# Kernel optimization log

Measured on AMD Instinct MI355X. Metric: run time of the kernel, lower is better.

## Reference

```python
import jax, jax.numpy as jnp
import numpy as np

K, D, O, B = 65536, 256, 256, 1024

def setup_inputs() -> dict:
    key = jax.random.key(0)
    k1, k2, k3 = jax.random.split(key, 3)
    return {
        "x": jax.random.normal(k1, (B, D), dtype=jnp.float32),
        "mean": jax.random.normal(k2, (K, D), dtype=jnp.float32),
        "stddev": jnp.ones((K, D), dtype=jnp.float32),
        "outputs": jax.random.normal(k3, (K, O), dtype=jnp.float32),
        "top_k": 32,
    }

def reference(x, mean, stddev, outputs, top_k):
    # Joint Gaussian log-prob summed over feature dim, computed without the
    # [B, K, D] broadcast torch materializes. Expanding sum_d ((x-mu)/sigma)^2
    # gives three GEMM-shaped terms.
    d = x.shape[-1]
    inv_var = 1.0 / (stddev * stddev)                      # [K, D]
    quad = ((x * x) @ inv_var.T                            # [B, K]
            - 2.0 * (x @ (mean * inv_var).T)
            + jnp.sum(mean * mean * inv_var, axis=-1))
    log_norm = jnp.sum(jnp.log(stddev), axis=-1) + 0.5 * d * jnp.log(2.0 * jnp.pi)
    joint_lp = -0.5 * quad - log_norm                      # [B, K]
    top_lp, top_idx = jax.lax.top_k(joint_lp, top_k)       # [B, top_k]
    weights = jax.nn.softmax(top_lp, axis=-1)              # [B, top_k]
    gathered = outputs[top_idx]                            # [B, top_k, O]
    return jnp.einsum('bko,bk->bo', gathered, weights)     # [B, O]
```

## Files before the change

### kernel.cpp

```cpp
#include <hip/hip_runtime.h>
#include <stdint.h>

#define KCOMP 65536
#define DDIM  256
#define ODIM  256
#define BROWS 1024
#define NCB   512
#define NBLK  512
#define LOG2PI_TERM 235.2482645f

typedef float f32x4 __attribute__((ext_vector_type(4)));
typedef __bf16 bf16x8 __attribute__((ext_vector_type(8)));
typedef unsigned int u32;
typedef unsigned long long u64;
typedef unsigned short u16;

typedef __attribute__((address_space(1))) const u32 gconst_u32;
typedef __attribute__((address_space(3))) u32 lds_u32;

__device__ __forceinline__ u16 f2bf(float f) {
  u32 b = __float_as_uint(f);
  b += 0x7FFFu + ((b >> 16) & 1u);
  return (u16)(b >> 16);
}
__device__ __forceinline__ u32 fkey(float f) {
  u32 b = __float_as_uint(f);
  return b ^ ((b >> 31) ? 0xFFFFFFFFu : 0x80000000u);
}

#define DPP_ROR1 0x121
#define DPP_ROR2 0x122
#define DPP_ROR4 0x124
#define DPP_ROR8 0x128

#define WS_A     0
#define WS_KEY   (1u << 20)

__global__ void prep_A(const float* __restrict__ x, u16* __restrict__ A) {
  int l = threadIdx.x & 63;
  int wv = threadIdx.x >> 6;
  int t = blockIdx.x;
  int row = t * 16 + (l & 15);
  for (int u = 0; u < 4; ++u) {
    int cc = wv * 4 + u;
    int d0 = cc * 16 + ((l >> 4) << 2);
    float4 xv = *(const float4*)(x + (size_t)row * DDIM + d0);
    float xs[4] = {xv.x, xv.y, xv.z, xv.w};
    uint4 v;
    u32 wds[4];
    for (int e = 0; e < 4; ++e)
      wds[e] = (u32)f2bf(xs[e] * xs[e]) | ((u32)f2bf(-2.0f * xs[e]) << 16);
    v.x = wds[0]; v.y = wds[1]; v.z = wds[2]; v.w = wds[3];
    *(uint4*)(A + ((size_t)(t * 16 + cc) * 64 + l) * 8) = v;
  }
}

__global__ __launch_bounds__(512, 4)
void main_gemm(const u16* __restrict__ A_ws, const float* __restrict__ mean,
               const float* __restrict__ stdd, u32* __restrict__ ckey) {
  __shared__ __align__(16) char lds_raw[66560];
  __shared__ u32 wsel[2][32][17];
  int tid = threadIdx.x, l = tid & 63, w = tid >> 6;
  int nb = blockIdx.x;
  int p = l & 15, q = l >> 4;

  u32 kid0 = (u32)(w * 16 + q * 4);

  bf16x8 wf[16];
  float myc0;
  f32x4 mycv;
  {
    u32* scr = (u32*)(lds_raw + w * 8320);
    int p8 = l & 7, q8 = l >> 3;
#pragma unroll
    for (int rr = 0; rr < 2; ++rr) {
      int comp = (nb * 8 + w) * 16 + rr * 8 + p8;
      const float* mrow = mean + (size_t)comp * DDIM + q8 * 32;
      const float* srow = stdd + (size_t)comp * DDIM + q8 * 32;
      float gsum = 0.f;
#pragma unroll
      for (int i = 0; i < 8; ++i) {
        float4 m4 = *(const float4*)(mrow + 4 * i);
        float4 s4 = *(const float4*)(srow + 4 * i);
        float ms[4] = {m4.x, m4.y, m4.z, m4.w};
        float ss[4] = {s4.x, s4.y, s4.z, s4.w};
        u32 wd[4];
#pragma unroll
        for (int e = 0; e < 4; ++e) {
          float iv = __builtin_amdgcn_rcpf(ss[e] * ss[e]);
          float miv = ms[e] * iv;
          wd[e] = (u32)f2bf(-0.5f * iv) | ((u32)f2bf(-0.5f * miv) << 16);
          gsum -= 0.5f * ms[e] * miv + __logf(ss[e]);
        }
        uint4 v; v.x = wd[0]; v.y = wd[1]; v.z = wd[2]; v.w = wd[3];
        *(uint4*)(scr + p8 * 260 + q8 * 32 + i * 4) = v;
      }
      gsum += __shfl_xor(gsum, 8);
      gsum += __shfl_xor(gsum, 16);
      gsum += __shfl_xor(gsum, 32);
      if ((p >> 3) == rr) {
        myc0 = gsum - LOG2PI_TERM;
#pragma unroll
        for (int cc = 0; cc < 16; ++cc)
          wf[cc] = *(const bf16x8*)(scr + (p & 7) * 260 + cc * 16 + q * 4);
      }
    }
#pragma unroll
    for (int i = 0; i < 4; ++i)
      mycv[i] = __shfl(myc0, q * 4 + i);
  }
  __syncthreads();

#define ASHP(B, CELL) (lds_raw + ((size_t)(B) * 32 + (CELL)) * 1024)

#define ISSUE(S, B)                                                           \
  {                                                                           \
    _Pragma("unroll")                                                         \
    for (int u = 0; u < 4; ++u) {                                             \
      int cell = w * 4 + u;                                                   \
      const u16* gsrc = A_ws +                                                \
        ((size_t)((S) * 2 + (cell >> 4)) * 16 + (cell & 15)) * 512            \
        + (size_t)l * 8;                                                      \
      __builtin_amdgcn_global_load_lds((gconst_u32*)gsrc,                     \
          (lds_u32*)ASHP(B, cell), 16, 0, 0);                                 \
    }                                                                         \
  }

#define MERGE_EMIT(ST, B)                                                     \
  {                                                                           \
    int r = tid;                                                              \
    u32 top[4] = {~0u, ~0u, ~0u, ~0u};                                        \
    _Pragma("unroll")                                                         \
    for (int j = 0; j < 16; ++j) {                                            \
      u32 key = wsel[B][r][j];                                                \
      if (key < top[3]) {                                                     \
        top[3] = key;                                                         \
        for (int z = 3; z > 0 && top[z] < top[z - 1]; --z) {                  \
          u32 tt = top[z]; top[z] = top[z - 1]; top[z - 1] = tt;              \
        }                                                                     \
      }                                                                       \
    }                                                                         \
    int rowg = (ST) * 32 + r;                                                 \
    uint4 ov; ov.x = ~top[0]; ov.y = ~top[1]; ov.z = ~top[2]; ov.w = ~top[3]; \
    *(uint4*)&ckey[((size_t)rowg * NCB + nb) * 4] = ov;                       \
  }

  ISSUE(0, 0)
  for (int s = 0; s < 32; ++s) {
    int pb = s & 1;
    __syncthreads();
    if (s < 31) ISSUE(s + 1, pb ^ 1)
    if (s > 0 && tid < 32) MERGE_EMIT(s - 1, pb ^ 1)

    f32x4 ac[2];
    ac[0] = mycv;
    ac[1] = mycv;
    __builtin_amdgcn_s_setprio(1);
#pragma unroll
    for (int cc = 0; cc < 16; ++cc) {
      bf16x8 a0 = *(const bf16x8*)(ASHP(pb, cc) + (size_t)l * 16);
      bf16x8 a1 = *(const bf16x8*)(ASHP(pb, 16 + cc) + (size_t)l * 16);
      ac[0] = __builtin_amdgcn_mfma_f32_16x16x32_bf16(wf[cc], a0, ac[0], 0, 0, 0);
      ac[1] = __builtin_amdgcn_mfma_f32_16x16x32_bf16(wf[cc], a1, ac[1], 0, 0, 0);
    }
    __builtin_amdgcn_s_setprio(0);

#define UMIN(a, b) ((a) < (b) ? (a) : (b))
#define UMAX(a, b) ((a) < (b) ? (b) : (a))
#pragma unroll
    for (int t = 0; t < 2; ++t) {
      u32 k0 = (__float_as_uint(ac[t][0]) & 0xFFFFFF00u) | (kid0 + 0);
      u32 k1 = (__float_as_uint(ac[t][1]) & 0xFFFFFF00u) | (kid0 + 1);
      u32 k2 = (__float_as_uint(ac[t][2]) & 0xFFFFFF00u) | (kid0 + 2);
      u32 k3 = (__float_as_uint(ac[t][3]) & 0xFFFFFF00u) | (kid0 + 3);
      u32 l0 = UMIN(k0, k1), h0 = UMAX(k0, k1);
      u32 l1 = UMIN(k2, k3), h1 = UMAX(k2, k3);
      u32 m1 = UMIN(l0, l1), m2 = UMIN(UMAX(l0, l1), UMIN(h0, h1));
      {
        u32 o1 = (u32)__shfl_xor((int)m1, 16);
        u32 o2 = (u32)__shfl_xor((int)m2, 16);
        u32 lo = UMIN(m1, o1), hi = UMAX(m1, o1), mn = UMIN(m2, o2);
        m1 = lo; m2 = UMIN(hi, mn);
      }
      {
        u32 o1 = (u32)__shfl_xor((int)m1, 32);
        u32 o2 = (u32)__shfl_xor((int)m2, 32);
        u32 lo = UMIN(m1, o1), hi = UMAX(m1, o1), mn = UMIN(m2, o2);
        m1 = lo; m2 = UMIN(hi, mn);
      }
      if (q == 0) {
        int r = t * 16 + p;
        wsel[pb][r][w * 2] = m1;
        wsel[pb][r][w * 2 + 1] = m2;
      }
    }
#undef UMIN
#undef UMAX
  }
  __syncthreads();
  if (tid < 32) MERGE_EMIT(31, 1)
#undef ISSUE
#undef MERGE_EMIT
#undef ASHP
}

__global__ __launch_bounds__(256)
void finalize(const float* __restrict__ x, const float* __restrict__ mean,
              const float* __restrict__ stdd, const float* __restrict__ outs,
              const u32* __restrict__ ckey, float* __restrict__ out) {
  __shared__ u32 cksh[2048];
  __shared__ float xr[256];
  __shared__ float part[256];
  __shared__ int selk[64];
  __shared__ float ew[32];
  __shared__ int kf[32];
  __shared__ float invs_sh;
  int tid = threadIdx.x, l = tid & 63, v = tid >> 6;
  int row = blockIdx.x;

  for (int i = tid; i < 2048; i += 256)
    cksh[i] = ckey[(size_t)row * 2048 + i];
  xr[tid] = x[(size_t)row * DDIM + tid];
  __syncthreads();

#define REDUCE_MAX(m)                                                         \
  {                                                                           \
    u32 o;                                                                    \
    o = (u32)__builtin_amdgcn_mov_dpp((int)m, DPP_ROR1, 0xf, 0xf, false);     \
    m = m > o ? m : o;                                                        \
    o = (u32)__builtin_amdgcn_mov_dpp((int)m, DPP_ROR2, 0xf, 0xf, false);     \
    m = m > o ? m : o;                                                        \
    o = (u32)__builtin_amdgcn_mov_dpp((int)m, DPP_ROR4, 0xf, 0xf, false);     \
    m = m > o ? m : o;                                                        \
    o = (u32)__builtin_amdgcn_mov_dpp((int)m, DPP_ROR8, 0xf, 0xf, false);     \
    m = m > o ? m : o;                                                        \
    o = (u32)__shfl_xor((int)m, 16); m = m > o ? m : o;                       \
    o = (u32)__shfl_xor((int)m, 32); m = m > o ? m : o;                       \
  }

  {
    u32 ext[8];
#pragma unroll
    for (int i = 0; i < 8; ++i) {
      int j = v * 512 + i * 64 + l;
      ext[i] = (cksh[j] & 0xFFFFFE00u) | ((u32)l << 3) | (u32)i;
    }
#define CSW(a, b) { if (ext[a] < ext[b]) { u32 t = ext[a]; ext[a] = ext[b]; ext[b] = t; } }
    CSW(0,1) CSW(2,3) CSW(4,5) CSW(6,7)
    CSW(0,2) CSW(1,3) CSW(4,6) CSW(5,7)
    CSW(1,2) CSW(5,6)
    CSW(0,4) CSW(1,5) CSW(2,6) CSW(3,7)
    CSW(2,4) CSW(3,5)
    CSW(1,2) CSW(3,4) CSW(5,6)
#undef CSW
    for (int it = 0; it < 16; ++it) {
      u32 m = ext[0];
      REDUCE_MAX(m)
      if (m == ext[0]) {
#pragma unroll
        for (int z = 0; z < 7; ++z) ext[z] = ext[z + 1];
        ext[7] = 0;
      }
      if (l == 0) {
        int wl = (int)((m >> 3) & 63u), wi = (int)(m & 7u);
        int j = v * 512 + wi * 64 + wl;
        selk[v * 16 + it] = (int)((u32)(j >> 2) * 128u + (~cksh[j] & 0x7Fu));
      }
    }
  }
  __syncthreads();

  {
    int j = tid >> 2, qq = tid & 3;
    int k = selk[j];
    const float* mr = mean + (size_t)k * DDIM + qq * 64;
    const float* sr = stdd + (size_t)k * DDIM + qq * 64;
    float s2 = 0.f, ls = 0.f;
    for (int i = 0; i < 16; ++i) {
      float4 m4 = *(const float4*)(mr + 4 * i);
      float4 s4 = *(const float4*)(sr + 4 * i);
      float4 x4 = *(const float4*)(&xr[qq * 64 + 4 * i]);
      { float is = 1.f / s4.x; float df = (x4.x - m4.x) * is; s2 += df * df; ls += __logf(s4.x); }
      { float is = 1.f / s4.y; float df = (x4.y - m4.y) * is; s2 += df * df; ls += __logf(s4.y); }
      { float is = 1.f / s4.z; float df = (x4.z - m4.z) * is; s2 += df * df; ls += __logf(s4.z); }
      { float is = 1.f / s4.w; float df = (x4.w - m4.w) * is; s2 += df * df; ls += __logf(s4.w); }
    }
    part[tid] = -0.5f * s2 - ls;
  }
  __syncthreads();

  if (tid < 64) {
    float lp0 = part[l * 4] + part[l * 4 + 1] + part[l * 4 + 2] +
                part[l * 4 + 3] - LOG2PI_TERM;
    u32 ext = (fkey(lp0) & 0xFFFFFFC0u) | (u32)l;
    float maxlp = 0.f, ssum = 0.f;
    for (int it = 0; it < 32; ++it) {
      u32 m = ext;
      REDUCE_MAX(m)
      int j = (int)(m & 63u);
      u32 vb = m & 0xFFFFFFC0u;
      vb ^= (vb >> 31) ? 0x80000000u : 0xFFFFFFFFu;
      float lp = __uint_as_float(vb);
      if (it == 0) maxlp = lp;
      float e = __expf(lp - maxlp);
      ssum += e;
      if (l == 0) { ew[it] = e; kf[it] = selk[j]; }
      if (j == l) ext = 0;
    }
    if (l == 0) invs_sh = 1.0f / ssum;
  }
  __syncthreads();
#undef REDUCE_MAX

  {
    float a = 0.f;
    for (int i = 0; i < 32; ++i)
      a += ew[i] * outs[(size_t)kf[i] * ODIM + tid];
    out[(size_t)row * ODIM + tid] = a * invs_sh;
  }
}

extern "C" void kernel_launch(void* const* d_in, const int* in_sizes, int n_in,
                              void* d_out, int out_size, void* d_ws, size_t ws_size,
                              hipStream_t stream) {
  const float* x = (const float*)d_in[0];
  const float* mean = (const float*)d_in[1];
  const float* stdd = (const float*)d_in[2];
  const float* outs = (const float*)d_in[3];
  char* ws = (char*)d_ws;
  u16* A_ws = (u16*)(ws + WS_A);
  u32* ckey = (u32*)(ws + WS_KEY);

  prep_A<<<64, 256, 0, stream>>>(x, A_ws);
  main_gemm<<<NBLK, 512, 0, stream>>>(A_ws, mean, stdd, ckey);
  finalize<<<BROWS, 256, 0, stream>>>(x, mean, stdd, outs, ckey,
                                      (float*)d_out);
}
```

Baseline: 379.7 us.

## Remap waves to 2x4 tile grid so each A fragment feeds two MFMAs

Waves are reorganised from 8 component groups times 2 row tiles into 2 row tiles times 4 component groups of 32 components each. Each wave now holds two sets of weight fragments and reuses one LDS A fragment for two MFMAs, halving LDS reads per MFMA. It also halves the per-row candidate count that the merge step scans. The cost is doubled weight-fragment registers, so launch bounds drop to 2 blocks per SM, lowering occupancy.

```diff
diff --git a/kernel.cpp b/kernel.cpp
--- a/kernel.cpp
+++ b/kernel.cpp
@@ -55,26 +55,29 @@
   }
 }
 
-__global__ __launch_bounds__(512, 4)
+__global__ __launch_bounds__(512, 2)
 void main_gemm(const u16* __restrict__ A_ws, const float* __restrict__ mean,
                const float* __restrict__ stdd, u32* __restrict__ ckey) {
   __shared__ __align__(16) char lds_raw[66560];
-  __shared__ u32 wsel[2][32][17];
+  __shared__ u32 wsel[2][32][9];
   int tid = threadIdx.x, l = tid & 63, w = tid >> 6;
   int nb = blockIdx.x;
   int p = l & 15, q = l >> 4;
-
-  u32 kid0 = (u32)(w * 16 + q * 4);
-
-  bf16x8 wf[16];
-  float myc0;
-  f32x4 mycv;
+  int wt = w >> 2;
+  int wc = w & 3;
+
+  u32 kid0 = (u32)(wc * 32 + q * 4);
+
+  bf16x8 wf[2][16];
+  float myc[2] = {0.f, 0.f};
+  f32x4 mycv[2];
   {
     u32* scr = (u32*)(lds_raw + w * 8320);
     int p8 = l & 7, q8 = l >> 3;
-#pragma unroll
-    for (int rr = 0; rr < 2; ++rr) {
-      int comp = (nb * 8 + w) * 16 + rr * 8 + p8;
+    int g0 = nb * 128 + wc * 32;
+#pragma unroll
+    for (int rr = 0; rr < 4; ++rr) {
+      int comp = g0 + rr * 8 + p8;
       const float* mrow = mean + (size_t)comp * DDIM + q8 * 32;
       const float* srow = stdd + (size_t)comp * DDIM + q8 * 32;
       float gsum = 0.f;
@@ -98,16 +101,21 @@
       gsum += __shfl_xor(gsum, 8);
       gsum += __shfl_xor(gsum, 16);
       gsum += __shfl_xor(gsum, 32);
-      if ((p >> 3) == rr) {
-        myc0 = gsum - LOG2PI_TERM;
-#pragma unroll
-        for (int cc = 0; cc < 16; ++cc)
-          wf[cc] = *(const bf16x8*)(scr + (p & 7) * 260 + cc * 16 + q * 4);
-      }
-    }
-#pragma unroll
-    for (int i = 0; i < 4; ++i)
-      mycv[i] = __shfl(myc0, q * 4 + i);
+#pragma unroll
+      for (int gs = 0; gs < 2; ++gs) {
+        if (((gs * 16 + p) >> 3) == rr) {
+          myc[gs] = gsum - LOG2PI_TERM;
+#pragma unroll
+          for (int cc = 0; cc < 16; ++cc)
+            wf[gs][cc] = *(const bf16x8*)(scr + (p & 7) * 260 + cc * 16 + q * 4);
+        }
+      }
+    }
+#pragma unroll
+    for (int gs = 0; gs < 2; ++gs)
+#pragma unroll
+      for (int i = 0; i < 4; ++i)
+        mycv[gs][i] = __shfl(myc[gs], q * 4 + i);
   }
   __syncthreads();
 
@@ -131,7 +139,7 @@
     int r = tid;                                                              \
     u32 top[4] = {~0u, ~0u, ~0u, ~0u};                                        \
     _Pragma("unroll")                                                         \
-    for (int j = 0; j < 16; ++j) {                                            \
+    for (int j = 0; j < 8; ++j) {                                             \
       u32 key = wsel[B][r][j];                                                \
       if (key < top[3]) {                                                     \
         top[3] = key;                                                         \
@@ -152,30 +160,43 @@
     if (s < 31) ISSUE(s + 1, pb ^ 1)
     if (s > 0 && tid < 32) MERGE_EMIT(s - 1, pb ^ 1)
 
-    f32x4 ac[2];
-    ac[0] = mycv;
-    ac[1] = mycv;
+    f32x4 ac0 = mycv[0];
+    f32x4 ac1 = mycv[1];
     __builtin_amdgcn_s_setprio(1);
 #pragma unroll
     for (int cc = 0; cc < 16; ++cc) {
-      bf16x8 a0 = *(const bf16x8*)(ASHP(pb, cc) + (size_t)l * 16);
-      bf16x8 a1 = *(const bf16x8*)(ASHP(pb, 16 + cc) + (size_t)l * 16);
-      ac[0] = __builtin_amdgcn_mfma_f32_16x16x32_bf16(wf[cc], a0, ac[0], 0, 0, 0);
-      ac[1] = __builtin_amdgcn_mfma_f32_16x16x32_bf16(wf[cc], a1, ac[1], 0, 0, 0);
+      bf16x8 a = *(const bf16x8*)(ASHP(pb, wt * 16 + cc) + (size_t)l * 16);
+      ac0 = __builtin_amdgcn_mfma_f32_16x16x32_bf16(wf[0][cc], a, ac0, 0, 0, 0);
+      ac1 = __builtin_amdgcn_mfma_f32_16x16x32_bf16(wf[1][cc], a, ac1, 0, 0, 0);
     }
     __builtin_amdgcn_s_setprio(0);
 
 #define UMIN(a, b) ((a) < (b) ? (a) : (b))
 #define UMAX(a, b) ((a) < (b) ? (b) : (a))
-#pragma unroll
-    for (int t = 0; t < 2; ++t) {
-      u32 k0 = (__float_as_uint(ac[t][0]) & 0xFFFFFF00u) | (kid0 + 0);
-      u32 k1 = (__float_as_uint(ac[t][1]) & 0xFFFFFF00u) | (kid0 + 1);
-      u32 k2 = (__float_as_uint(ac[t][2]) & 0xFFFFFF00u) | (kid0 + 2);
-      u32 k3 = (__float_as_uint(ac[t][3]) & 0xFFFFFF00u) | (kid0 + 3);
-      u32 l0 = UMIN(k0, k1), h0 = UMAX(k0, k1);
-      u32 l1 = UMIN(k2, k3), h1 = UMAX(k2, k3);
-      u32 m1 = UMIN(l0, l1), m2 = UMIN(UMAX(l0, l1), UMIN(h0, h1));
+    {
+      u32 a1_, a2_, b1_, b2_;
+      {
+        u32 k0 = (__float_as_uint(ac0[0]) & 0xFFFFFF00u) | (kid0 + 0);
+        u32 k1 = (__float_as_uint(ac0[1]) & 0xFFFFFF00u) | (kid0 + 1);
+        u32 k2 = (__float_as_uint(ac0[2]) & 0xFFFFFF00u) | (kid0 + 2);
+        u32 k3 = (__float_as_uint(ac0[3]) & 0xFFFFFF00u) | (kid0 + 3);
+        u32 l0 = UMIN(k0, k1), h0 = UMAX(k0, k1);
+        u32 l1 = UMIN(k2, k3), h1 = UMAX(k2, k3);
+        a1_ = UMIN(l0, l1);
+        a2_ = UMIN(UMAX(l0, l1), UMIN(h0, h1));
+      }
+      {
+        u32 k0 = (__float_as_uint(ac1[0]) & 0xFFFFFF00u) | (kid0 + 16);
+        u32 k1 = (__float_as_uint(ac1[1]) & 0xFFFFFF00u) | (kid0 + 17);
+        u32 k2 = (__float_as_uint(ac1[2]) & 0xFFFFFF00u) | (kid0 + 18);
+        u32 k3 = (__float_as_uint(ac1[3]) & 0xFFFFFF00u) | (kid0 + 19);
+        u32 l0 = UMIN(k0, k1), h0 = UMAX(k0, k1);
+        u32 l1 = UMIN(k2, k3), h1 = UMAX(k2, k3);
+        b1_ = UMIN(l0, l1);
+        b2_ = UMIN(UMAX(l0, l1), UMIN(h0, h1));
+      }
+      u32 m1 = UMIN(a1_, b1_);
+      u32 m2 = UMIN(UMAX(a1_, b1_), UMIN(a2_, b2_));
       {
         u32 o1 = (u32)__shfl_xor((int)m1, 16);
         u32 o2 = (u32)__shfl_xor((int)m2, 16);
@@ -189,9 +210,9 @@
         m1 = lo; m2 = UMIN(hi, mn);
       }
       if (q == 0) {
-        int r = t * 16 + p;
-        wsel[pb][r][w * 2] = m1;
-        wsel[pb][r][w * 2 + 1] = m2;
+        int r = wt * 16 + p;
+        wsel[pb][r][wc * 2] = m1;
+        wsel[pb][r][wc * 2 + 1] = m2;
       }
     }
 #undef UMIN
```

Result: slower. 391.1 us (+3.0%).

## Read GEMM A tiles directly from global memory instead of LDS double-buffering

Applied to the files above, without the earlier changes.

Removes the global_load_lds double-buffered staging of the component A tiles and has each wave load its bf16x8 MFMA operands straight from global memory (through L2/L1), replacing __syncthreads with a lighter lgkmcnt wait plus s_barrier. This drops the LDS traffic and full-block sync per stage, but loses explicit prefetch overlap, so MFMA issue may stall on global-load latency. The finalize kernel also swaps exact division for the hardware reciprocal approximation.

```diff
diff --git a/kernel.cpp b/kernel.cpp
--- a/kernel.cpp
+++ b/kernel.cpp
@@ -14,9 +14,6 @@
 typedef unsigned int u32;
 typedef unsigned long long u64;
 typedef unsigned short u16;
-
-typedef __attribute__((address_space(1))) const u32 gconst_u32;
-typedef __attribute__((address_space(3))) u32 lds_u32;
 
 __device__ __forceinline__ u16 f2bf(float f) {
   u32 b = __float_as_uint(f);
@@ -110,21 +107,6 @@
       mycv[i] = __shfl(myc0, q * 4 + i);
   }
   __syncthreads();
-
-#define ASHP(B, CELL) (lds_raw + ((size_t)(B) * 32 + (CELL)) * 1024)
-
-#define ISSUE(S, B)                                                           \
-  {                                                                           \
-    _Pragma("unroll")                                                         \
-    for (int u = 0; u < 4; ++u) {                                             \
-      int cell = w * 4 + u;                                                   \
-      const u16* gsrc = A_ws +                                                \
-        ((size_t)((S) * 2 + (cell >> 4)) * 16 + (cell & 15)) * 512            \
-        + (size_t)l * 8;                                                      \
-      __builtin_amdgcn_global_load_lds((gconst_u32*)gsrc,                     \
-          (lds_u32*)ASHP(B, cell), 16, 0, 0);                                 \
-    }                                                                         \
-  }
 
 #define MERGE_EMIT(ST, B)                                                     \
   {                                                                           \
@@ -145,12 +127,14 @@
     *(uint4*)&ckey[((size_t)rowg * NCB + nb) * 4] = ov;                       \
   }
 
-  ISSUE(0, 0)
   for (int s = 0; s < 32; ++s) {
     int pb = s & 1;
-    __syncthreads();
-    if (s < 31) ISSUE(s + 1, pb ^ 1)
+    asm volatile("s_waitcnt lgkmcnt(0)" ::: "memory");
+    __builtin_amdgcn_s_barrier();
+    asm volatile("" ::: "memory");
     if (s > 0 && tid < 32) MERGE_EMIT(s - 1, pb ^ 1)
+
+    const u16* As = A_ws + (size_t)s * 16384;
 
     f32x4 ac[2];
     ac[0] = mycv;
@@ -158,8 +142,8 @@
     __builtin_amdgcn_s_setprio(1);
 #pragma unroll
     for (int cc = 0; cc < 16; ++cc) {
-      bf16x8 a0 = *(const bf16x8*)(ASHP(pb, cc) + (size_t)l * 16);
-      bf16x8 a1 = *(const bf16x8*)(ASHP(pb, 16 + cc) + (size_t)l * 16);
+      bf16x8 a0 = *(const bf16x8*)(As + (size_t)cc * 512 + (size_t)l * 8);
+      bf16x8 a1 = *(const bf16x8*)(As + 8192 + (size_t)cc * 512 + (size_t)l * 8);
       ac[0] = __builtin_amdgcn_mfma_f32_16x16x32_bf16(wf[cc], a0, ac[0], 0, 0, 0);
       ac[1] = __builtin_amdgcn_mfma_f32_16x16x32_bf16(wf[cc], a1, ac[1], 0, 0, 0);
     }
@@ -199,9 +183,7 @@
   }
   __syncthreads();
   if (tid < 32) MERGE_EMIT(31, 1)
-#undef ISSUE
 #undef MERGE_EMIT
-#undef ASHP
 }
 
 __global__ __launch_bounds__(256)
@@ -280,10 +262,10 @@
       float4 m4 = *(const float4*)(mr + 4 * i);
       float4 s4 = *(const float4*)(sr + 4 * i);
       float4 x4 = *(const float4*)(&xr[qq * 64 + 4 * i]);
-      { float is = 1.f / s4.x; float df = (x4.x - m4.x) * is; s2 += df * df; ls += __logf(s4.x); }
-      { float is = 1.f / s4.y; float df = (x4.y - m4.y) * is; s2 += df * df; ls += __logf(s4.y); }
-      { float is = 1.f / s4.z; float df = (x4.z - m4.z) * is; s2 += df * df; ls += __logf(s4.z); }
-      { float is = 1.f / s4.w; float df = (x4.w - m4.w) * is; s2 += df * df; ls += __logf(s4.w); }
+      { float is = __builtin_amdgcn_rcpf(s4.x); float df = (x4.x - m4.x) * is; s2 += df * df; ls += __logf(s4.x); }
+      { float is = __builtin_amdgcn_rcpf(s4.y); float df = (x4.y - m4.y) * is; s2 += df * df; ls += __logf(s4.y); }
+      { float is = __builtin_amdgcn_rcpf(s4.z); float df = (x4.z - m4.z) * is; s2 += df * df; ls += __logf(s4.z); }
+      { float is = __builtin_amdgcn_rcpf(s4.w); float df = (x4.w - m4.w) * is; s2 += df * df; ls += __logf(s4.w); }
     }
     part[tid] = -0.5f * s2 - ls;
   }
```

After: 387.5 us. +2.0%, slower.

## Split GEMM waves across row tiles and K halves, double block count

Applied to the files above, without the earlier changes.

The main GEMM now uses 1024 blocks of 64 components each instead of 512 blocks of 128. The eight waves split as two row tiles times four component groups, and each wave covers only half of the D reduction in each of two accumulators, which are summed afterward. Per-block candidate output shrinks from top-4 to top-2 per row, which halves the merge work, and finalize decodes indices accordingly. Finalize also swaps the exact reciprocal for the fast rcp intrinsic. The changes aim for more parallelism and shorter per-wave MFMA chains, at the cost of extra prologue loads of mean/stddev per block and a top-2 candidate set per 64 components. That candidate set could affect exactness of the top-32 selection.

```diff
diff --git a/kernel.cpp b/kernel.cpp
--- a/kernel.cpp
+++ b/kernel.cpp
@@ -5,8 +5,7 @@
 #define DDIM  256
 #define ODIM  256
 #define BROWS 1024
-#define NCB   512
-#define NBLK  512
+#define NCB   1024
 #define LOG2PI_TERM 235.2482645f
 
 typedef float f32x4 __attribute__((ext_vector_type(4)));
@@ -59,12 +58,14 @@
 void main_gemm(const u16* __restrict__ A_ws, const float* __restrict__ mean,
                const float* __restrict__ stdd, u32* __restrict__ ckey) {
   __shared__ __align__(16) char lds_raw[66560];
-  __shared__ u32 wsel[2][32][17];
+  __shared__ u32 wsel[2][32][9];
   int tid = threadIdx.x, l = tid & 63, w = tid >> 6;
   int nb = blockIdx.x;
   int p = l & 15, q = l >> 4;
-
-  u32 kid0 = (u32)(w * 16 + q * 4);
+  int rt = w >> 2;
+  int cg = w & 3;
+
+  u32 kid0 = (u32)(cg * 16 + q * 4);
 
   bf16x8 wf[16];
   float myc0;
@@ -74,7 +75,7 @@
     int p8 = l & 7, q8 = l >> 3;
 #pragma unroll
     for (int rr = 0; rr < 2; ++rr) {
-      int comp = (nb * 8 + w) * 16 + rr * 8 + p8;
+      int comp = (nb * 4 + cg) * 16 + rr * 8 + p8;
       const float* mrow = mean + (size_t)comp * DDIM + q8 * 32;
       const float* srow = stdd + (size_t)comp * DDIM + q8 * 32;
       float gsum = 0.f;
@@ -129,20 +130,16 @@
 #define MERGE_EMIT(ST, B)                                                     \
   {                                                                           \
     int r = tid;                                                              \
-    u32 top[4] = {~0u, ~0u, ~0u, ~0u};                                        \
+    u32 b1 = ~0u, b2 = ~0u;                                                   \
     _Pragma("unroll")                                                         \
-    for (int j = 0; j < 16; ++j) {                                            \
+    for (int j = 0; j < 8; ++j) {                                             \
       u32 key = wsel[B][r][j];                                                \
-      if (key < top[3]) {                                                     \
-        top[3] = key;                                                         \
-        for (int z = 3; z > 0 && top[z] < top[z - 1]; --z) {                  \
-          u32 tt = top[z]; top[z] = top[z - 1]; top[z - 1] = tt;              \
-        }                                                                     \
-      }                                                                       \
+      if (key < b1) { b2 = b1; b1 = key; }                                    \
+      else if (key < b2) { b2 = key; }                                        \
     }                                                                         \
     int rowg = (ST) * 32 + r;                                                 \
-    uint4 ov; ov.x = ~top[0]; ov.y = ~top[1]; ov.z = ~top[2]; ov.w = ~top[3]; \
-    *(uint4*)&ckey[((size_t)rowg * NCB + nb) * 4] = ov;                       \
+    uint2 ov; ov.x = ~b1; ov.y = ~b2;                                         \
+    *(uint2*)&ckey[((size_t)rowg * NCB + nb) * 2] = ov;                       \
   }
 
   ISSUE(0, 0)
@@ -152,27 +149,28 @@
     if (s < 31) ISSUE(s + 1, pb ^ 1)
     if (s > 0 && tid < 32) MERGE_EMIT(s - 1, pb ^ 1)
 
-    f32x4 ac[2];
-    ac[0] = mycv;
-    ac[1] = mycv;
+    f32x4 aca = mycv;
+    f32x4 acb = (f32x4){0.f, 0.f, 0.f, 0.f};
     __builtin_amdgcn_s_setprio(1);
 #pragma unroll
-    for (int cc = 0; cc < 16; ++cc) {
-      bf16x8 a0 = *(const bf16x8*)(ASHP(pb, cc) + (size_t)l * 16);
-      bf16x8 a1 = *(const bf16x8*)(ASHP(pb, 16 + cc) + (size_t)l * 16);
-      ac[0] = __builtin_amdgcn_mfma_f32_16x16x32_bf16(wf[cc], a0, ac[0], 0, 0, 0);
-      ac[1] = __builtin_amdgcn_mfma_f32_16x16x32_bf16(wf[cc], a1, ac[1], 0, 0, 0);
+    for (int cc = 0; cc < 8; ++cc) {
+      bf16x8 a0 = *(const bf16x8*)(ASHP(pb, rt * 16 + cc) + (size_t)l * 16);
+      bf16x8 a1 = *(const bf16x8*)(ASHP(pb, rt * 16 + 8 + cc) + (size_t)l * 16);
+      aca = __builtin_amdgcn_mfma_f32_16x16x32_bf16(wf[cc], a0, aca, 0, 0, 0);
+      acb = __builtin_amdgcn_mfma_f32_16x16x32_bf16(wf[8 + cc], a1, acb, 0, 0, 0);
     }
     __builtin_amdgcn_s_setprio(0);
+    f32x4 ac;
+    ac[0] = aca[0] + acb[0]; ac[1] = aca[1] + acb[1];
+    ac[2] = aca[2] + acb[2]; ac[3] = aca[3] + acb[3];
 
 #define UMIN(a, b) ((a) < (b) ? (a) : (b))
 #define UMAX(a, b) ((a) < (b) ? (b) : (a))
-#pragma unroll
-    for (int t = 0; t < 2; ++t) {
-      u32 k0 = (__float_as_uint(ac[t][0]) & 0xFFFFFF00u) | (kid0 + 0);
-      u32 k1 = (__float_as_uint(ac[t][1]) & 0xFFFFFF00u) | (kid0 + 1);
-      u32 k2 = (__float_as_uint(ac[t][2]) & 0xFFFFFF00u) | (kid0 + 2);
-      u32 k3 = (__float_as_uint(ac[t][3]) & 0xFFFFFF00u) | (kid0 + 3);
+    {
+      u32 k0 = (__float_as_uint(ac[0]) & 0xFFFFFF00u) | (kid0 + 0);
+      u32 k1 = (__float_as_uint(ac[1]) & 0xFFFFFF00u) | (kid0 + 1);
+      u32 k2 = (__float_as_uint(ac[2]) & 0xFFFFFF00u) | (kid0 + 2);
+      u32 k3 = (__float_as_uint(ac[3]) & 0xFFFFFF00u) | (kid0 + 3);
       u32 l0 = UMIN(k0, k1), h0 = UMAX(k0, k1);
       u32 l1 = UMIN(k2, k3), h1 = UMAX(k2, k3);
       u32 m1 = UMIN(l0, l1), m2 = UMIN(UMAX(l0, l1), UMIN(h0, h1));
@@ -189,9 +187,9 @@
         m1 = lo; m2 = UMIN(hi, mn);
       }
       if (q == 0) {
-        int r = t * 16 + p;
-        wsel[pb][r][w * 2] = m1;
-        wsel[pb][r][w * 2 + 1] = m2;
+        int r = rt * 16 + p;
+        wsel[pb][r][cg * 2] = m1;
+        wsel[pb][r][cg * 2 + 1] = m2;
       }
     }
 #undef UMIN
@@ -264,7 +262,7 @@
       if (l == 0) {
         int wl = (int)((m >> 3) & 63u), wi = (int)(m & 7u);
         int j = v * 512 + wi * 64 + wl;
-        selk[v * 16 + it] = (int)((u32)(j >> 2) * 128u + (~cksh[j] & 0x7Fu));
+        selk[v * 16 + it] = (int)((u32)(j >> 1) * 64u + (~cksh[j] & 0x3Fu));
       }
     }
   }
@@ -280,10 +278,10 @@
       float4 m4 = *(const float4*)(mr + 4 * i);
       float4 s4 = *(const float4*)(sr + 4 * i);
       float4 x4 = *(const float4*)(&xr[qq * 64 + 4 * i]);
-      { float is = 1.f / s4.x; float df = (x4.x - m4.x) * is; s2 += df * df; ls += __logf(s4.x); }
-      { float is = 1.f / s4.y; float df = (x4.y - m4.y) * is; s2 += df * df; ls += __logf(s4.y); }
-      { float is = 1.f / s4.z; float df = (x4.z - m4.z) * is; s2 += df * df; ls += __logf(s4.z); }
-      { float is = 1.f / s4.w; float df = (x4.w - m4.w) * is; s2 += df * df; ls += __logf(s4.w); }
+      { float is = __builtin_amdgcn_rcpf(s4.x); float df = (x4.x - m4.x) * is; s2 += df * df; ls += __logf(s4.x); }
+      { float is = __builtin_amdgcn_rcpf(s4.y); float df = (x4.y - m4.y) * is; s2 += df * df; ls += __logf(s4.y); }
+      { float is = __builtin_amdgcn_rcpf(s4.z); float df = (x4.z - m4.z) * is; s2 += df * df; ls += __logf(s4.z); }
+      { float is = __builtin_amdgcn_rcpf(s4.w); float df = (x4.w - m4.w) * is; s2 += df * df; ls += __logf(s4.w); }
     }
     part[tid] = -0.5f * s2 - ls;
   }
@@ -332,7 +330,7 @@
   u32* ckey = (u32*)(ws + WS_KEY);
 
   prep_A<<<64, 256, 0, stream>>>(x, A_ws);
-  main_gemm<<<NBLK, 512, 0, stream>>>(A_ws, mean, stdd, ckey);
+  main_gemm<<<NCB, 512, 0, stream>>>(A_ws, mean, stdd, ckey);
   finalize<<<BROWS, 256, 0, stream>>>(x, mean, stdd, outs, ckey,
                                       (float*)d_out);
 }
```

Result: faster. 338.8 us (-10.8%).
